# Kernel tuning notes

Hardware: AMD Instinct MI355X
Metric: run time of the kernel (lower is better)

Reference implementation:

```python
import jax, jax.numpy as jnp
import numpy as np

N = 50000      # nodes
E = 800000     # edges (avg degree 16)
DIN = 256      # input_dim
H = 4          # heads
C = 32         # output_dim per head
HID = H * C    # 128
NEG_SLOPE = 0.2


def setup_inputs() -> dict:
    key = jax.random.key(0)
    ks = jax.random.split(key, 12)
    s = 0.05
    d = {}
    d["x"] = jax.random.normal(ks[0], (N, DIN), jnp.float32)
    d["edge_index"] = jax.random.randint(ks[1], (2, E), 0, N, jnp.int32)
    # GATv2Conv layer 0 (in=DIN)
    d["Wl0"] = jax.random.normal(ks[2], (HID, DIN), jnp.float32) * s
    d["Wr0"] = jax.random.normal(ks[3], (HID, DIN), jnp.float32) * s
    d["att0"] = jax.random.normal(ks[4], (H, C), jnp.float32) * s
    d["b0"] = jnp.zeros((HID,), jnp.float32)
    # GATv2Conv layer 1 (in=HID)
    d["Wl1"] = jax.random.normal(ks[5], (HID, HID), jnp.float32) * s
    d["Wr1"] = jax.random.normal(ks[6], (HID, HID), jnp.float32) * s
    d["att1"] = jax.random.normal(ks[7], (H, C), jnp.float32) * s
    d["b1"] = jnp.zeros((HID,), jnp.float32)
    # down_proj: Linear(HID -> C)
    d["down_W"] = jax.random.normal(ks[8], (C, HID), jnp.float32) * s
    d["down_b"] = jnp.zeros((C,), jnp.float32)
    return d


def _gatv2_layer(x, src, dst, Wl, Wr, att, b, n):
    # x: [n, Din]; src/dst: [Etot] (self loops included)
    xl = (x @ Wl.T).reshape(n, H, C)   # messages (x_j side, lin_l)
    xr = (x @ Wr.T).reshape(n, H, C)   # target side (x_i, lin_r)
    e = jax.nn.leaky_relu(xl[src] + xr[dst], NEG_SLOPE)   # [Etot, H, C]
    logits = jnp.einsum('ehc,hc->eh', e, att)             # [Etot, H]
    # softmax over incoming edges per destination node
    m = jax.ops.segment_max(logits, dst, num_segments=n)
    ex = jnp.exp(logits - m[dst])
    den = jax.ops.segment_sum(ex, dst, num_segments=n)
    alpha = ex / den[dst]                                 # [Etot, H]
    out = jax.ops.segment_sum(alpha[:, :, None] * xl[src], dst, num_segments=n)
    return out.reshape(n, HID) + b                        # concat heads + bias


def reference(x, edge_index, Wl0, Wr0, att0, b0, Wl1, Wr1, att1, b1, down_W, down_b):
    n = x.shape[0]
    loops = jnp.arange(n, dtype=edge_index.dtype)
    ei = jnp.concatenate([edge_index, jnp.stack([loops, loops])], axis=1)  # add_self_loops=True
    src, dst = ei[0], ei[1]
    h = _gatv2_layer(x, src, dst, Wl0, Wr0, att0, b0, n)
    h = _gatv2_layer(h, src, dst, Wl1, Wr1, att1, b1, n)
    return h @ down_W.T + down_b    # down_proj: [n, C]
```

## Files before the change

kernel.cpp:

```cpp
#include <hip/hip_runtime.h>

#define CAP 64
#define BCAP 6144

typedef _Float16 h8 __attribute__((ext_vector_type(8)));
typedef _Float16 h4 __attribute__((ext_vector_type(4)));
typedef _Float16 h2 __attribute__((ext_vector_type(2)));
typedef float f32x4 __attribute__((ext_vector_type(4)));

__device__ __forceinline__ float lrelu(float x){ return x > 0.f ? x : 0.2f * x; }
__device__ __forceinline__ uint4 pack8(float4 a, float4 b){
  union { h8 h; uint4 u; } cv;
  cv.h = (h8){ (_Float16)a.x, (_Float16)a.y, (_Float16)a.z, (_Float16)a.w,
               (_Float16)b.x, (_Float16)b.y, (_Float16)b.z, (_Float16)b.w };
  return cv.u;
}

__device__ __forceinline__ float edge_logit(uint4 xu, const h2* xrh, const h2* avh){
  union { uint4 u; h2 v[4]; } cu; cu.u = xu;
  const h2 z2 = { (_Float16)0.f, (_Float16)0.f };
  const h2 sl = { (_Float16)0.2f, (_Float16)0.2f };
  float p = 0.f;
  #pragma unroll
  for (int k = 0; k < 4; ++k){
    h2 t  = cu.v[k] + xrh[k];
    h2 hi = __builtin_elementwise_max(t, z2);
    h2 lo = __builtin_elementwise_min(t, z2);
    h2 lr = hi + lo * sl;
    p = __builtin_amdgcn_fdot2(lr, avh[k], p, false);
  }
  return p;
}
__device__ __forceinline__ void acc_edge(float w, uint4 xu, float* accv){
  union { uint4 u; _Float16 e[8]; } ce; ce.u = xu;
  #pragma unroll
  for (int i = 0; i < 8; ++i) accv[i] += w * (float)ce.e[i];
}

__global__ void convw_kernel(const float* __restrict__ Wl0, const float* __restrict__ Wr0,
                             const float* __restrict__ Wl1, const float* __restrict__ Wr1,
                             _Float16* __restrict__ B0h, _Float16* __restrict__ B1h){
  int t = blockIdx.x * blockDim.x + threadIdx.x;
  const float* s; _Float16* d; int off;
  if (t < 8192)      { s = Wl0; d = B0h;          off = t; }
  else if (t < 16384){ s = Wr0; d = B0h + 32768;  off = t - 8192; }
  else if (t < 20480){ s = Wl1; d = B1h;          off = t - 16384; }
  else               { s = Wr1; d = B1h + 16384;  off = t - 20480; }
  float4 f = ((const float4*)s)[off];
  h4 h = { (_Float16)f.x, (_Float16)f.y, (_Float16)f.z, (_Float16)f.w };
  *(h4*)(d + 4 * (size_t)off) = h;
}

__global__ void scatter_kernel(const int* __restrict__ cnt, const int* __restrict__ hist,
                               int* __restrict__ cursor, int* __restrict__ perm, int n){
  __shared__ int base[64];
  __shared__ int lh[64];
  __shared__ int lbase[64];
  __shared__ int ht[64];
  if (threadIdx.x < 64){
    lh[threadIdx.x] = 0;
    ht[threadIdx.x] = hist[threadIdx.x];
  }
  __syncthreads();
  if (threadIdx.x == 0){
    int acc = 0;
    for (int d = 63; d >= 0; --d){ base[d] = acc; acc += ht[d]; }
  }
  int i = blockIdx.x * blockDim.x + threadIdx.x;
  int d = 1, lr = 0;
  if (i < n){
    d = cnt[i]; d = (d < 1) ? 1 : (d > CAP ? CAP : d);
    lr = atomicAdd(&lh[d - 1], 1);
  }
  __syncthreads();
  if (threadIdx.x < 64 && lh[threadIdx.x] > 0)
    lbase[threadIdx.x] = atomicAdd(&cursor[threadIdx.x], lh[threadIdx.x]);
  __syncthreads();
  if (i < n)
    perm[base[d - 1] + lbase[d - 1] + lr] = i;
}

__device__ __forceinline__ void gemm_body(
    char* smem, const float* __restrict__ A32, const _Float16* __restrict__ A16,
    const _Float16* __restrict__ Bw, _Float16* __restrict__ C, int n, int K,
    int bx, int by)
{
  char* Abase = smem;
  char* Bbase = smem + 8192;

  const int tid  = threadIdx.x;
  const int lane = tid & 63;
  const int wx   = tid >> 6;
  const int r0   = by * 64;
  const int cb   = bx * 128;
  const int m16  = lane & 15, quad = lane >> 4;

  f32x4 acc[4][2];
  #pragma unroll
  for (int i = 0; i < 4; ++i)
    #pragma unroll
    for (int j = 0; j < 2; ++j)
      acc[i][j] = (f32x4){0.f, 0.f, 0.f, 0.f};

  const int srow = tid >> 2;
  const int kq   = (tid & 3) << 4;
  const int kb   = kq * 2;
  const int swz  = (srow & 7) << 4;

  uint4 ra[2], rb[2][2];
  const uint4 z = {0u, 0u, 0u, 0u};

  if (r0 + srow < n){
    if (A32){
      const float* p = A32 + (size_t)(r0 + srow) * K + kq;
      ra[0] = pack8(*(const float4*)(p),     *(const float4*)(p + 4));
      ra[1] = pack8(*(const float4*)(p + 8), *(const float4*)(p + 12));
    } else {
      const _Float16* p = A16 + (size_t)(r0 + srow) * K + kq;
      ra[0] = *(const uint4*)(p);
      ra[1] = *(const uint4*)(p + 8);
    }
  } else { ra[0] = z; ra[1] = z; }
  #pragma unroll
  for (int v = 0; v < 2; ++v){
    const _Float16* p = Bw + (size_t)(cb + v * 64 + srow) * K + kq;
    rb[v][0] = *(const uint4*)(p);
    rb[v][1] = *(const uint4*)(p + 8);
  }

  const int nt = K >> 6;
  for (int t = 0; t < nt; ++t){
    *(uint4*)(Abase + srow * 128 + (kb ^ swz))        = ra[0];
    *(uint4*)(Abase + srow * 128 + ((kb + 16) ^ swz)) = ra[1];
    #pragma unroll
    for (int v = 0; v < 2; ++v){
      *(uint4*)(Bbase + (v * 64 + srow) * 128 + (kb ^ swz))        = rb[v][0];
      *(uint4*)(Bbase + (v * 64 + srow) * 128 + ((kb + 16) ^ swz)) = rb[v][1];
    }
    __syncthreads();
    if (t + 1 < nt){
      int kt = (t + 1) << 6;
      if (r0 + srow < n){
        if (A32){
          const float* p = A32 + (size_t)(r0 + srow) * K + kt + kq;
          ra[0] = pack8(*(const float4*)(p),     *(const float4*)(p + 4));
          ra[1] = pack8(*(const float4*)(p + 8), *(const float4*)(p + 12));
        } else {
          const _Float16* p = A16 + (size_t)(r0 + srow) * K + kt + kq;
          ra[0] = *(const uint4*)(p);
          ra[1] = *(const uint4*)(p + 8);
        }
      }
      #pragma unroll
      for (int v = 0; v < 2; ++v){
        const _Float16* p = Bw + (size_t)(cb + v * 64 + srow) * K + kt + kq;
        rb[v][0] = *(const uint4*)(p);
        rb[v][1] = *(const uint4*)(p + 8);
      }
    }
    const int swr = (m16 & 7) << 4;
    #pragma unroll
    for (int ks = 0; ks < 2; ++ks){
      const int k0 = ks * 32 + quad * 8;
      const int cbyte = (k0 * 2) ^ swr;
      h8 a[4], b[2];
      #pragma unroll
      for (int i = 0; i < 4; ++i)
        a[i] = *(const h8*)(Abase + (i * 16 + m16) * 128 + cbyte);
      #pragma unroll
      for (int j = 0; j < 2; ++j)
        b[j] = *(const h8*)(Bbase + (wx * 32 + j * 16 + m16) * 128 + cbyte);
      #pragma unroll
      for (int i = 0; i < 4; ++i)
        #pragma unroll
        for (int j = 0; j < 2; ++j)
          acc[i][j] = __builtin_amdgcn_mfma_f32_16x16x32_f16(a[i], b[j], acc[i][j], 0, 0, 0);
    }
    __syncthreads();
  }

  _Float16* Csm = (_Float16*)smem;
  #pragma unroll
  for (int i = 0; i < 4; ++i)
    #pragma unroll
    for (int r = 0; r < 4; ++r){
      int lrow = i * 16 + quad * 4 + r;
      _Float16* cp = Csm + lrow * 136 + wx * 32 + m16;
      #pragma unroll
      for (int j = 0; j < 2; ++j)
        cp[j * 16] = (_Float16)acc[i][j][r];
    }
  __syncthreads();
  #pragma unroll
  for (int v = 0; v < 4; ++v){
    int idx = v * 256 + tid;
    int row = idx >> 4, cx = (idx & 15) * 8;
    if (r0 + row < n)
      *(uint4*)(C + (size_t)(r0 + row) * 256 + cb + cx)
        = *(const uint4*)(Csm + row * 136 + cx);
  }
}

__global__ __launch_bounds__(256) void gemm_mfma(
    const float* __restrict__ A32, const _Float16* __restrict__ A16,
    const _Float16* __restrict__ Bw, _Float16* __restrict__ C, int n, int K)
{
  __shared__ __align__(16) char smem[24576];
  gemm_body(smem, A32, A16, Bw, C, n, K, blockIdx.x, blockIdx.y);
}

__global__ __launch_bounds__(256) void gemm_pass1(
    const float* __restrict__ A32, const _Float16* __restrict__ Bw,
    _Float16* __restrict__ C, int n,
    const int* __restrict__ ei, int* __restrict__ bins, int* __restrict__ bcursor,
    int e_orig, int etot, int NP)
{
  __shared__ __align__(16) char smem[24576];
  const int lin = blockIdx.x;
  if (lin >= NP){
    int gi = lin - NP;
    gemm_body(smem, A32, nullptr, Bw, C, n, 256, gi & 1, gi >> 1);
  } else {
    int* lcnt  = (int*)smem;
    int* gbase = lcnt + 256;
    const int tid = threadIdx.x;
    if (tid < 196) lcnt[tid] = 0;
    __syncthreads();
    const int base = lin * 2048 + tid;
    int pk[8], bk[8], lp[8];
    #pragma unroll
    for (int k = 0; k < 8; ++k){
      int i = base + k * 256;
      bk[k] = -1;
      if (i < etot){
        int src, dst;
        if (i < e_orig){ src = ei[i]; dst = ei[e_orig + i]; }
        else { src = i - e_orig; dst = src; }
        bk[k] = dst >> 8;
        pk[k] = ((dst & 255) << 24) | src;
      }
    }
    #pragma unroll
    for (int k = 0; k < 8; ++k)
      if (bk[k] >= 0) lp[k] = atomicAdd(&lcnt[bk[k]], 1);
    __syncthreads();
    if (tid < 196 && lcnt[tid] > 0)
      gbase[tid] = atomicAdd(&bcursor[tid], lcnt[tid]);
    __syncthreads();
    #pragma unroll
    for (int k = 0; k < 8; ++k)
      if (bk[k] >= 0){
        int p = gbase[bk[k]] + lp[k];
        if (p < BCAP) bins[(size_t)bk[k] * BCAP + p] = pk[k];
      }
  }
}

__global__ __launch_bounds__(256) void pass2_kernel(
    const int* __restrict__ bins, const int* __restrict__ bcursor,
    int* __restrict__ cnt, int* __restrict__ col2, int* __restrict__ hist, int n)
{
  __shared__ int stage[256 * CAP];
  __shared__ int lcnt2[256];
  __shared__ int lh[64];
  const int b = blockIdx.x, tid = threadIdx.x;
  lcnt2[tid] = 0;
  if (tid < 64) lh[tid] = 0;
  __syncthreads();
  int ecnt = bcursor[b]; if (ecnt > BCAP) ecnt = BCAP;
  for (int i = tid; i < ecnt; i += 256){
    int v = bins[(size_t)b * BCAP + i];
    int src = v & 0xFFFFFF;
    int loc = ((unsigned)v) >> 24;
    int pos = atomicAdd(&lcnt2[loc], 1);
    if (pos < CAP) stage[loc * CAP + pos] = src;
  }
  __syncthreads();
  int node = b * 256 + tid;
  if (node < n){
    int d = lcnt2[tid];
    cnt[node] = d;
    int dc = d < 1 ? 1 : (d > CAP ? CAP : d);
    atomicAdd(&lh[dc - 1], 1);
  }
  __syncthreads();
  const uint4* sg = (const uint4*)stage;
  uint4* c4 = (uint4*)col2;
  for (int k2 = tid; k2 < 4096; k2 += 256){
    int nd = b * 256 + (k2 >> 4);
    if (nd < n) c4[(size_t)nd * 16 + (k2 & 15)] = sg[k2];
  }
  if (tid < 64 && lh[tid] > 0) atomicAdd(&hist[tid], lh[tid]);
}

__global__ __launch_bounds__(128) void agg_wave(
    const _Float16* __restrict__ XLR, const int* __restrict__ col2,
    const int* __restrict__ cnt, const int* __restrict__ perm,
    const float* __restrict__ att,
    const float* __restrict__ bias, _Float16* __restrict__ H16, int n)
{
  __shared__ int idxs[8][72];
  const int lane  = threadIdx.x & 63;
  const int g     = lane >> 4;
  const int ll    = lane & 15;
  const int gbase = g << 4;
  const int nl    = ((threadIdx.x >> 6) << 2) + g;
  const int slot  = blockIdx.x * 8 + nl;
  if (slot >= n) return;
  const int node = perm[slot];
  int deg = cnt[node]; if (deg > CAP) deg = CAP;
  const int c0 = 8 * ll;

  h2 xrh[4], avh[4];
  {
    union { uint4 u; h2 v[4]; } xc;
    xc.u = *(const uint4*)(XLR + (size_t)node * 256 + 128 + c0);
    #pragma unroll
    for (int k = 0; k < 4; ++k) xrh[k] = xc.v[k];
    #pragma unroll
    for (int k = 0; k < 4; ++k)
      avh[k] = (h2){ (_Float16)att[c0 + 2*k], (_Float16)att[c0 + 2*k + 1] };
  }

  {
    int sq[4];
    #pragma unroll
    for (int q = 0; q < 4; ++q)
      sq[q] = (ll + 16*q < deg) ? col2[(size_t)node * CAP + ll + 16*q] : 0;
    int s0 = __shfl(sq[0], gbase);
    #pragma unroll
    for (int q = 0; q < 4; ++q)
      idxs[nl][ll + 16*q] = (ll + 16*q < deg) ? sq[q] : s0;
    if (ll < 8) idxs[nl][64 + ll] = s0;
  }
  const int* idxp = idxs[nl];

  float l = 0.f, accv[8];
  #pragma unroll
  for (int i = 0; i < 8; ++i) accv[i] = 0.f;

  uint4 x0, x1, x2, x3, x4, x5, x6, x7;
  {
    int e0 = idxp[0], e1 = idxp[1], e2 = idxp[2], e3 = idxp[3];
    int e4 = idxp[4], e5 = idxp[5], e6 = idxp[6], e7 = idxp[7];
    x0 = *(const uint4*)(XLR + (size_t)e0 * 256 + c0);
    x1 = *(const uint4*)(XLR + (size_t)e1 * 256 + c0);
    x2 = *(const uint4*)(XLR + (size_t)e2 * 256 + c0);
    x3 = *(const uint4*)(XLR + (size_t)e3 * 256 + c0);
    x4 = *(const uint4*)(XLR + (size_t)e4 * 256 + c0);
    x5 = *(const uint4*)(XLR + (size_t)e5 * 256 + c0);
    x6 = *(const uint4*)(XLR + (size_t)e6 * 256 + c0);
    x7 = *(const uint4*)(XLR + (size_t)e7 * 256 + c0);
  }

  int j = 0;
  for (; j + 4 <= deg; j += 4){
    uint4 y0 = x0, y1 = x1, y2 = x2, y3 = x3;
    x0 = x4; x1 = x5; x2 = x6; x3 = x7;
    int e8  = idxp[j + 8],  e9  = idxp[j + 9];
    int e10 = idxp[j + 10], e11 = idxp[j + 11];
    x4 = *(const uint4*)(XLR + (size_t)e8  * 256 + c0);
    x5 = *(const uint4*)(XLR + (size_t)e9  * 256 + c0);
    x6 = *(const uint4*)(XLR + (size_t)e10 * 256 + c0);
    x7 = *(const uint4*)(XLR + (size_t)e11 * 256 + c0);
    float p0 = edge_logit(y0, xrh, avh);
    float p1 = edge_logit(y1, xrh, avh);
    float p2 = edge_logit(y2, xrh, avh);
    float p3 = edge_logit(y3, xrh, avh);
    p0 += __shfl_xor(p0, 1);  p1 += __shfl_xor(p1, 1);
    p2 += __shfl_xor(p2, 1);  p3 += __shfl_xor(p3, 1);
    p0 += __shfl_xor(p0, 2);  p1 += __shfl_xor(p1, 2);
    p2 += __shfl_xor(p2, 2);  p3 += __shfl_xor(p3, 2);
    float w0 = __expf(p0), w1 = __expf(p1), w2 = __expf(p2), w3 = __expf(p3);
    l += (w0 + w1) + (w2 + w3);
    acc_edge(w0, y0, accv); acc_edge(w1, y1, accv);
    acc_edge(w2, y2, accv); acc_edge(w3, y3, accv);
  }
  #pragma unroll
  for (int r = 0; r < 3; ++r){
    if (j + r < deg){
      uint4 xe = (r == 0) ? x0 : ((r == 1) ? x1 : x2);
      float p = edge_logit(xe, xrh, avh);
      p += __shfl_xor(p, 1);
      p += __shfl_xor(p, 2);
      float w = __expf(p);
      l += w;
      acc_edge(w, xe, accv);
    }
  }
  float inv = 1.f / l;
  union { h8 h; uint4 u; } o;
  #pragma unroll
  for (int i = 0; i < 8; ++i)
    o.h[i] = (_Float16)(accv[i] * inv + bias[c0 + i]);
  *(uint4*)(H16 + (size_t)node * 128 + c0) = o.u;
}

__global__ __launch_bounds__(256) void agg_down(
    const _Float16* __restrict__ XLR, const int* __restrict__ col2,
    const int* __restrict__ cnt, const int* __restrict__ perm,
    const float* __restrict__ att,
    const float* __restrict__ bias, const float* __restrict__ dW,
    const float* __restrict__ db, float* __restrict__ out, int n)
{
  __shared__ float dwb[32][129];
  __shared__ float hsm[16][128];
  __shared__ int idxs[16][72];
  for (int i = threadIdx.x; i < 32 * 128; i += 256)
    dwb[i >> 7][i & 127] = dW[i];

  const int lane  = threadIdx.x & 63;
  const int g     = lane >> 4;
  const int ll    = lane & 15;
  const int gbase = g << 4;
  const int nl    = ((threadIdx.x >> 6) << 2) + g;
  const int slot  = blockIdx.x * 16 + nl;
  const bool valid = slot < n;
  const int node = valid ? perm[slot] : 0;
  int deg = 0;
  if (valid){ deg = cnt[node]; if (deg > CAP) deg = CAP; }
  const int c0 = 8 * ll;

  h2 xrh[4], avh[4];
  {
    union { uint4 u; h2 v[4]; } xc;
    xc.u = (uint4){0u,0u,0u,0u};
    if (valid) xc.u = *(const uint4*)(XLR + (size_t)node * 256 + 128 + c0);
    #pragma unroll
    for (int k = 0; k < 4; ++k) xrh[k] = xc.v[k];
    #pragma unroll
    for (int k = 0; k < 4; ++k)
      avh[k] = (h2){ (_Float16)att[c0 + 2*k], (_Float16)att[c0 + 2*k + 1] };
  }

  {
    int sq[4];
    #pragma unroll
    for (int q = 0; q < 4; ++q)
      sq[q] = (valid && ll + 16*q < deg) ? col2[(size_t)node * CAP + ll + 16*q] : 0;
    int s0 = __shfl(sq[0], gbase);
    #pragma unroll
    for (int q = 0; q < 4; ++q)
      idxs[nl][ll + 16*q] = (ll + 16*q < deg) ? sq[q] : s0;
    if (ll < 8) idxs[nl][64 + ll] = s0;
  }
  const int* idxp = idxs[nl];

  float l = 0.f, accv[8];
  #pragma unroll
  for (int i = 0; i < 8; ++i) accv[i] = 0.f;

  uint4 x0, x1, x2, x3, x4, x5, x6, x7;
  {
    int e0 = idxp[0], e1 = idxp[1], e2 = idxp[2], e3 = idxp[3];
    int e4 = idxp[4], e5 = idxp[5], e6 = idxp[6], e7 = idxp[7];
    x0 = *(const uint4*)(XLR + (size_t)e0 * 256 + c0);
    x1 = *(const uint4*)(XLR + (size_t)e1 * 256 + c0);
    x2 = *(const uint4*)(XLR + (size_t)e2 * 256 + c0);
    x3 = *(const uint4*)(XLR + (size_t)e3 * 256 + c0);
    x4 = *(const uint4*)(XLR + (size_t)e4 * 256 + c0);
    x5 = *(const uint4*)(XLR + (size_t)e5 * 256 + c0);
    x6 = *(const uint4*)(XLR + (size_t)e6 * 256 + c0);
    x7 = *(const uint4*)(XLR + (size_t)e7 * 256 + c0);
  }

  int j = 0;
  for (; j + 4 <= deg; j += 4){
    uint4 y0 = x0, y1 = x1, y2 = x2, y3 = x3;
    x0 = x4; x1 = x5; x2 = x6; x3 = x7;
    int e8  = idxp[j + 8],  e9  = idxp[j + 9];
    int e10 = idxp[j + 10], e11 = idxp[j + 11];
    x4 = *(const uint4*)(XLR + (size_t)e8  * 256 + c0);
    x5 = *(const uint4*)(XLR + (size_t)e9  * 256 + c0);
    x6 = *(const uint4*)(XLR + (size_t)e10 * 256 + c0);
    x7 = *(const uint4*)(XLR + (size_t)e11 * 256 + c0);
    float p0 = edge_logit(y0, xrh, avh);
    float p1 = edge_logit(y1, xrh, avh);
    float p2 = edge_logit(y2, xrh, avh);
    float p3 = edge_logit(y3, xrh, avh);
    p0 += __shfl_xor(p0, 1);  p1 += __shfl_xor(p1, 1);
    p2 += __shfl_xor(p2, 1);  p3 += __shfl_xor(p3, 1);
    p0 += __shfl_xor(p0, 2);  p1 += __shfl_xor(p1, 2);
    p2 += __shfl_xor(p2, 2);  p3 += __shfl_xor(p3, 2);
    float w0 = __expf(p0), w1 = __expf(p1), w2 = __expf(p2), w3 = __expf(p3);
    l += (w0 + w1) + (w2 + w3);
    acc_edge(w0, y0, accv); acc_edge(w1, y1, accv);
    acc_edge(w2, y2, accv); acc_edge(w3, y3, accv);
  }
  #pragma unroll
  for (int r = 0; r < 3; ++r){
    if (j + r < deg){
      uint4 xe = (r == 0) ? x0 : ((r == 1) ? x1 : x2);
      float p = edge_logit(xe, xrh, avh);
      p += __shfl_xor(p, 1);
      p += __shfl_xor(p, 2);
      float w = __expf(p);
      l += w;
      acc_edge(w, xe, accv);
    }
  }
  {
    float inv = (deg > 0) ? 1.f / l : 0.f;
    #pragma unroll
    for (int i = 0; i < 8; ++i)
      hsm[nl][c0 + i] = accv[i] * inv + bias[c0 + i];
  }
  __syncthreads();

  const int o = threadIdx.x & 31;
  #pragma unroll
  for (int h2i = 0; h2i < 2; ++h2i){
    int nl2 = (threadIdx.x >> 5) + h2i * 8;
    int slot2 = blockIdx.x * 16 + nl2;
    float sum = 0.f;
    #pragma unroll 8
    for (int k = 0; k < 128; ++k)
      sum += hsm[nl2][k] * dwb[o][k];
    if (slot2 < n)
      out[(size_t)perm[slot2] * 32 + o] = sum + db[o];
  }
}

extern "C" void kernel_launch(void* const* d_in, const int* in_sizes, int n_in,
                              void* d_out, int out_size, void* d_ws, size_t ws_size,
                              hipStream_t stream) {
  const float* x     = (const float*)d_in[0];
  const int*   ei    = (const int*)  d_in[1];
  const float* Wl0   = (const float*)d_in[2];
  const float* Wr0   = (const float*)d_in[3];
  const float* att0  = (const float*)d_in[4];
  const float* b0    = (const float*)d_in[5];
  const float* Wl1   = (const float*)d_in[6];
  const float* Wr1   = (const float*)d_in[7];
  const float* att1  = (const float*)d_in[8];
  const float* b1    = (const float*)d_in[9];
  const float* dW    = (const float*)d_in[10];
  const float* db    = (const float*)d_in[11];
  float* out = (float*)d_out;

  const int n    = in_sizes[0] / 256;
  const int e    = in_sizes[1] / 2;
  const int etot = e + n;

  _Float16* XLR16 = (_Float16*)d_ws;
  _Float16* H16   = XLR16 + (size_t)n * 256;
  int* col2 = (int*)(H16 + (size_t)n * 128);
  int* cnt  = col2 + (size_t)n * CAP;
  int* hist    = cnt + n;
  int* cursor  = hist + 64;
  int* bcursor = cursor + 64;
  int* perm    = bcursor + 256;
  _Float16* B0h = (_Float16*)(perm + ((n + 3) & ~3));
  _Float16* B1h = B0h + 65536;
  int* bins = (int*)H16;

  (void)hipMemsetAsync(cnt, 0, ((size_t)n + 384) * sizeof(int), stream);
  convw_kernel<<<96, 256, 0, stream>>>(Wl0, Wr0, Wl1, Wr1, B0h, B1h);

  const int NP = (etot + 2047) / 2048;
  const int NG = 2 * ((n + 63) / 64);
  gemm_pass1<<<NP + NG, 256, 0, stream>>>(x, B0h, XLR16, n, ei, bins, bcursor,
                                          e, etot, NP);

  const int NB2 = (n + 255) / 256;
  pass2_kernel<<<NB2, 256, 0, stream>>>(bins, bcursor, cnt, col2, hist, n);
  scatter_kernel<<<(n + 255) / 256, 256, 0, stream>>>(cnt, hist, cursor, perm, n);

  agg_wave<<<(n + 7) / 8, 128, 0, stream>>>(XLR16, col2, cnt, perm, att0, b0, H16, n);
  dim3 ggrid(2, (n + 63) / 64);
  gemm_mfma<<<ggrid, 256, 0, stream>>>(nullptr, H16, B1h, XLR16, n, 128);
  agg_down<<<(n + 15) / 16, 256, 0, stream>>>(XLR16, col2, cnt, perm, att1, b1, dW, db, out, n);
}
```

Measured before the change: 274.5 us.

## Fuse layer-0 aggregation with layer-1 GEMM in permuted slot order

Replaces the separate layer-0 aggregation kernel and layer-1 GEMM with a single kernel that aggregates 64 nodes into shared memory and multiplies them by the layer-1 weights with MFMA. The H16 intermediate round-trip and one launch go away. The layer-1 features are now stored in degree-sorted slot order, so an inverse permutation is built in the scatter kernel and used by the second aggregation to remap neighbour indices. The fused kernel uses about 53KB of shared memory, which lowers occupancy, and the second aggregation pays an extra indirect load per edge.

```diff
diff --git a/kernel.cpp b/kernel.cpp
--- a/kernel.cpp
+++ b/kernel.cpp
@@ -8,7 +8,6 @@
 typedef _Float16 h2 __attribute__((ext_vector_type(2)));
 typedef float f32x4 __attribute__((ext_vector_type(4)));
 
-__device__ __forceinline__ float lrelu(float x){ return x > 0.f ? x : 0.2f * x; }
 __device__ __forceinline__ uint4 pack8(float4 a, float4 b){
   union { h8 h; uint4 u; } cv;
   cv.h = (h8){ (_Float16)a.x, (_Float16)a.y, (_Float16)a.z, (_Float16)a.w,
@@ -52,7 +51,8 @@
 }
 
 __global__ void scatter_kernel(const int* __restrict__ cnt, const int* __restrict__ hist,
-                               int* __restrict__ cursor, int* __restrict__ perm, int n){
+                               int* __restrict__ cursor, int* __restrict__ perm,
+                               int* __restrict__ iperm, int n){
   __shared__ int base[64];
   __shared__ int lh[64];
   __shared__ int lbase[64];
@@ -76,12 +76,15 @@
   if (threadIdx.x < 64 && lh[threadIdx.x] > 0)
     lbase[threadIdx.x] = atomicAdd(&cursor[threadIdx.x], lh[threadIdx.x]);
   __syncthreads();
-  if (i < n)
-    perm[base[d - 1] + lbase[d - 1] + lr] = i;
+  if (i < n){
+    int pos = base[d - 1] + lbase[d - 1] + lr;
+    perm[pos] = i;
+    iperm[i] = pos;
+  }
 }
 
 __device__ __forceinline__ void gemm_body(
-    char* smem, const float* __restrict__ A32, const _Float16* __restrict__ A16,
+    char* smem, const float* __restrict__ A32,
     const _Float16* __restrict__ Bw, _Float16* __restrict__ C, int n, int K,
     int bx, int by)
 {
@@ -111,15 +114,9 @@
   const uint4 z = {0u, 0u, 0u, 0u};
 
   if (r0 + srow < n){
-    if (A32){
-      const float* p = A32 + (size_t)(r0 + srow) * K + kq;
-      ra[0] = pack8(*(const float4*)(p),     *(const float4*)(p + 4));
-      ra[1] = pack8(*(const float4*)(p + 8), *(const float4*)(p + 12));
-    } else {
-      const _Float16* p = A16 + (size_t)(r0 + srow) * K + kq;
-      ra[0] = *(const uint4*)(p);
-      ra[1] = *(const uint4*)(p + 8);
-    }
+    const float* p = A32 + (size_t)(r0 + srow) * K + kq;
+    ra[0] = pack8(*(const float4*)(p),     *(const float4*)(p + 4));
+    ra[1] = pack8(*(const float4*)(p + 8), *(const float4*)(p + 12));
   } else { ra[0] = z; ra[1] = z; }
   #pragma unroll
   for (int v = 0; v < 2; ++v){
@@ -141,15 +138,9 @@
     if (t + 1 < nt){
       int kt = (t + 1) << 6;
       if (r0 + srow < n){
-        if (A32){
-          const float* p = A32 + (size_t)(r0 + srow) * K + kt + kq;
-          ra[0] = pack8(*(const float4*)(p),     *(const float4*)(p + 4));
-          ra[1] = pack8(*(const float4*)(p + 8), *(const float4*)(p + 12));
-        } else {
-          const _Float16* p = A16 + (size_t)(r0 + srow) * K + kt + kq;
-          ra[0] = *(const uint4*)(p);
-          ra[1] = *(const uint4*)(p + 8);
-        }
+        const float* p = A32 + (size_t)(r0 + srow) * K + kt + kq;
+        ra[0] = pack8(*(const float4*)(p),     *(const float4*)(p + 4));
+        ra[1] = pack8(*(const float4*)(p + 8), *(const float4*)(p + 12));
       }
       #pragma unroll
       for (int v = 0; v < 2; ++v){
@@ -199,14 +190,6 @@
       *(uint4*)(C + (size_t)(r0 + row) * 256 + cb + cx)
         = *(const uint4*)(Csm + row * 136 + cx);
   }
-}
-
-__global__ __launch_bounds__(256) void gemm_mfma(
-    const float* __restrict__ A32, const _Float16* __restrict__ A16,
-    const _Float16* __restrict__ Bw, _Float16* __restrict__ C, int n, int K)
-{
-  __shared__ __align__(16) char smem[24576];
-  gemm_body(smem, A32, A16, Bw, C, n, K, blockIdx.x, blockIdx.y);
 }
 
 __global__ __launch_bounds__(256) void gemm_pass1(
@@ -219,7 +202,7 @@
   const int lin = blockIdx.x;
   if (lin >= NP){
     int gi = lin - NP;
-    gemm_body(smem, A32, nullptr, Bw, C, n, 256, gi & 1, gi >> 1);
+    gemm_body(smem, A32, Bw, C, n, 256, gi & 1, gi >> 1);
   } else {
     int* lcnt  = (int*)smem;
     int* gbase = lcnt + 256;
@@ -293,112 +276,210 @@
   if (tid < 64 && lh[tid] > 0) atomicAdd(&hist[tid], lh[tid]);
 }
 
-__global__ __launch_bounds__(128) void agg_wave(
+__global__ __launch_bounds__(256) void agg_gemm1(
     const _Float16* __restrict__ XLR, const int* __restrict__ col2,
     const int* __restrict__ cnt, const int* __restrict__ perm,
-    const float* __restrict__ att,
-    const float* __restrict__ bias, _Float16* __restrict__ H16, int n)
+    const float* __restrict__ att, const float* __restrict__ bias,
+    const _Float16* __restrict__ B1h, _Float16* __restrict__ XLR1, int n)
 {
-  __shared__ int idxs[8][72];
-  const int lane  = threadIdx.x & 63;
-  const int g     = lane >> 4;
-  const int ll    = lane & 15;
-  const int gbase = g << 4;
-  const int nl    = ((threadIdx.x >> 6) << 2) + g;
-  const int slot  = blockIdx.x * 8 + nl;
-  if (slot >= n) return;
-  const int node = perm[slot];
-  int deg = cnt[node]; if (deg > CAP) deg = CAP;
+  __shared__ __align__(16) char smem[53760];
+  char* Hs = smem;
+  char* Bs = smem + 16384;
+  int (*idxs)[72] = (int(*)[72])(smem + 49152);
+
+  const int tid  = threadIdx.x;
+  const int lane = tid & 63;
+  const int g = lane >> 4, ll = lane & 15, gbase = g << 4;
+  const int nlq = ((tid >> 6) << 2) + g;
+  const int slot0 = blockIdx.x * 64;
   const int c0 = 8 * ll;
 
-  h2 xrh[4], avh[4];
+  for (int rnd = 0; rnd < 4; ++rnd){
+    const int lrow = rnd * 16 + nlq;
+    const int slot = slot0 + lrow;
+    const bool valid = slot < n;
+    const int node = valid ? perm[slot] : 0;
+    int deg = 0;
+    if (valid){ deg = cnt[node]; if (deg > CAP) deg = CAP; }
+
+    h2 xrh[4], avh[4];
+    {
+      union { uint4 u; h2 v[4]; } xc;
+      xc.u = (uint4){0u,0u,0u,0u};
+      if (valid) xc.u = *(const uint4*)(XLR + (size_t)node * 256 + 128 + c0);
+      #pragma unroll
+      for (int k = 0; k < 4; ++k) xrh[k] = xc.v[k];
+      #pragma unroll
+      for (int k = 0; k < 4; ++k)
+        avh[k] = (h2){ (_Float16)att[c0 + 2*k], (_Float16)att[c0 + 2*k + 1] };
+    }
+    {
+      int sq[4];
+      #pragma unroll
+      for (int q = 0; q < 4; ++q)
+        sq[q] = (valid && ll + 16*q < deg) ? col2[(size_t)node * CAP + ll + 16*q] : 0;
+      int s0 = __shfl(sq[0], gbase);
+      #pragma unroll
+      for (int q = 0; q < 4; ++q)
+        idxs[nlq][ll + 16*q] = (ll + 16*q < deg) ? sq[q] : s0;
+      if (ll < 8) idxs[nlq][64 + ll] = s0;
+    }
+    const int* idxp = idxs[nlq];
+
+    float l = 0.f, accv[8];
+    #pragma unroll
+    for (int i = 0; i < 8; ++i) accv[i] = 0.f;
+
+    uint4 x0, x1, x2, x3, x4, x5, x6, x7;
+    {
+      int e0 = idxp[0], e1 = idxp[1], e2 = idxp[2], e3 = idxp[3];
+      int e4 = idxp[4], e5 = idxp[5], e6 = idxp[6], e7 = idxp[7];
+      x0 = *(const uint4*)(XLR + (size_t)e0 * 256 + c0);
+      x1 = *(const uint4*)(XLR + (size_t)e1 * 256 + c0);
+      x2 = *(const uint4*)(XLR + (size_t)e2 * 256 + c0);
+      x3 = *(const uint4*)(XLR + (size_t)e3 * 256 + c0);
+      x4 = *(const uint4*)(XLR + (size_t)e4 * 256 + c0);
+      x5 = *(const uint4*)(XLR + (size_t)e5 * 256 + c0);
+      x6 = *(const uint4*)(XLR + (size_t)e6 * 256 + c0);
+      x7 = *(const uint4*)(XLR + (size_t)e7 * 256 + c0);
+    }
+
+    int j = 0;
+    for (; j + 4 <= deg; j += 4){
+      uint4 y0 = x0, y1 = x1, y2 = x2, y3 = x3;
+      x0 = x4; x1 = x5; x2 = x6; x3 = x7;
+      int e8  = idxp[j + 8],  e9  = idxp[j + 9];
+      int e10 = idxp[j + 10], e11 = idxp[j + 11];
+      x4 = *(const uint4*)(XLR + (size_t)e8  * 256 + c0);
+      x5 = *(const uint4*)(XLR + (size_t)e9  * 256 + c0);
+      x6 = *(const uint4*)(XLR + (size_t)e10 * 256 + c0);
+      x7 = *(const uint4*)(XLR + (size_t)e11 * 256 + c0);
+      float p0 = edge_logit(y0, xrh, avh);
+      float p1 = edge_logit(y1, xrh, avh);
+      float p2 = edge_logit(y2, xrh, avh);
+      float p3 = edge_logit(y3, xrh, avh);
+      p0 += __shfl_xor(p0, 1);  p1 += __shfl_xor(p1, 1);
+      p2 += __shfl_xor(p2, 1);  p3 += __shfl_xor(p3, 1);
+      p0 += __shfl_xor(p0, 2);  p1 += __shfl_xor(p1, 2);
+      p2 += __shfl_xor(p2, 2);  p3 += __shfl_xor(p3, 2);
+      float w0 = __expf(p0), w1 = __expf(p1), w2 = __expf(p2), w3 = __expf(p3);
+      l += (w0 + w1) + (w2 + w3);
+      acc_edge(w0, y0, accv); acc_edge(w1, y1, accv);
+      acc_edge(w2, y2, accv); acc_edge(w3, y3, accv);
+    }
+    #pragma unroll
+    for (int r = 0; r < 3; ++r){
+      if (j + r < deg){
+        uint4 xe = (r == 0) ? x0 : ((r == 1) ? x1 : x2);
+        float p = edge_logit(xe, xrh, avh);
+        p += __shfl_xor(p, 1);
+        p += __shfl_xor(p, 2);
+        float w = __expf(p);
+        l += w;
+        acc_edge(w, xe, accv);
+      }
+    }
+    if (valid){
+      float inv = (deg > 0) ? 1.f / l : 0.f;
+      union { h8 h; uint4 u; } o;
+      #pragma unroll
+      for (int i = 0; i < 8; ++i)
+        o.h[i] = (_Float16)(accv[i] * inv + bias[c0 + i]);
+      *(uint4*)(Hs + lrow * 256 + ((c0 * 2) ^ ((lrow & 7) << 4))) = o.u;
+    }
+  }
+  __syncthreads();
+
+  const int wx = tid >> 6;
+  const int m16 = lane & 15, quad = lane >> 4;
+  const int swr = (m16 & 7) << 4;
+  f32x4 acc[4][4];
+  #pragma unroll
+  for (int i = 0; i < 4; ++i)
+    #pragma unroll
+    for (int j = 0; j < 4; ++j)
+      acc[i][j] = (f32x4){0.f, 0.f, 0.f, 0.f};
+
+  uint4 rbf[8];
   {
-    union { uint4 u; h2 v[4]; } xc;
-    xc.u = *(const uint4*)(XLR + (size_t)node * 256 + 128 + c0);
-    #pragma unroll
-    for (int k = 0; k < 4; ++k) xrh[k] = xc.v[k];
-    #pragma unroll
-    for (int k = 0; k < 4; ++k)
-      avh[k] = (h2){ (_Float16)att[c0 + 2*k], (_Float16)att[c0 + 2*k + 1] };
-  }
-
+    const _Float16* p = B1h + (size_t)tid * 128;
+    #pragma unroll
+    for (int k = 0; k < 8; ++k) rbf[k] = *(const uint4*)(p + k * 8);
+  }
+  #pragma unroll
+  for (int k = 0; k < 8; ++k)
+    *(uint4*)(Bs + tid * 128 + ((k * 16) ^ ((tid & 7) << 4))) = rbf[k];
+  __syncthreads();
   {
-    int sq[4];
-    #pragma unroll
-    for (int q = 0; q < 4; ++q)
-      sq[q] = (ll + 16*q < deg) ? col2[(size_t)node * CAP + ll + 16*q] : 0;
-    int s0 = __shfl(sq[0], gbase);
-    #pragma unroll
-    for (int q = 0; q < 4; ++q)
-      idxs[nl][ll + 16*q] = (ll + 16*q < deg) ? sq[q] : s0;
-    if (ll < 8) idxs[nl][64 + ll] = s0;
-  }
-  const int* idxp = idxs[nl];
-
-  float l = 0.f, accv[8];
-  #pragma unroll
-  for (int i = 0; i < 8; ++i) accv[i] = 0.f;
-
-  uint4 x0, x1, x2, x3, x4, x5, x6, x7;
-  {
-    int e0 = idxp[0], e1 = idxp[1], e2 = idxp[2], e3 = idxp[3];
-    int e4 = idxp[4], e5 = idxp[5], e6 = idxp[6], e7 = idxp[7];
-    x0 = *(const uint4*)(XLR + (size_t)e0 * 256 + c0);
-    x1 = *(const uint4*)(XLR + (size_t)e1 * 256 + c0);
-    x2 = *(const uint4*)(XLR + (size_t)e2 * 256 + c0);
-    x3 = *(const uint4*)(XLR + (size_t)e3 * 256 + c0);
-    x4 = *(const uint4*)(XLR + (size_t)e4 * 256 + c0);
-    x5 = *(const uint4*)(XLR + (size_t)e5 * 256 + c0);
-    x6 = *(const uint4*)(XLR + (size_t)e6 * 256 + c0);
-    x7 = *(const uint4*)(XLR + (size_t)e7 * 256 + c0);
-  }
-
-  int j = 0;
-  for (; j + 4 <= deg; j += 4){
-    uint4 y0 = x0, y1 = x1, y2 = x2, y3 = x3;
-    x0 = x4; x1 = x5; x2 = x6; x3 = x7;
-    int e8  = idxp[j + 8],  e9  = idxp[j + 9];
-    int e10 = idxp[j + 10], e11 = idxp[j + 11];
-    x4 = *(const uint4*)(XLR + (size_t)e8  * 256 + c0);
-    x5 = *(const uint4*)(XLR + (size_t)e9  * 256 + c0);
-    x6 = *(const uint4*)(XLR + (size_t)e10 * 256 + c0);
-    x7 = *(const uint4*)(XLR + (size_t)e11 * 256 + c0);
-    float p0 = edge_logit(y0, xrh, avh);
-    float p1 = edge_logit(y1, xrh, avh);
-    float p2 = edge_logit(y2, xrh, avh);
-    float p3 = edge_logit(y3, xrh, avh);
-    p0 += __shfl_xor(p0, 1);  p1 += __shfl_xor(p1, 1);
-    p2 += __shfl_xor(p2, 1);  p3 += __shfl_xor(p3, 1);
-    p0 += __shfl_xor(p0, 2);  p1 += __shfl_xor(p1, 2);
-    p2 += __shfl_xor(p2, 2);  p3 += __shfl_xor(p3, 2);
-    float w0 = __expf(p0), w1 = __expf(p1), w2 = __expf(p2), w3 = __expf(p3);
-    l += (w0 + w1) + (w2 + w3);
-    acc_edge(w0, y0, accv); acc_edge(w1, y1, accv);
-    acc_edge(w2, y2, accv); acc_edge(w3, y3, accv);
-  }
-  #pragma unroll
-  for (int r = 0; r < 3; ++r){
-    if (j + r < deg){
-      uint4 xe = (r == 0) ? x0 : ((r == 1) ? x1 : x2);
-      float p = edge_logit(xe, xrh, avh);
-      p += __shfl_xor(p, 1);
-      p += __shfl_xor(p, 2);
-      float w = __expf(p);
-      l += w;
-      acc_edge(w, xe, accv);
-    }
-  }
-  float inv = 1.f / l;
-  union { h8 h; uint4 u; } o;
-  #pragma unroll
-  for (int i = 0; i < 8; ++i)
-    o.h[i] = (_Float16)(accv[i] * inv + bias[c0 + i]);
-  *(uint4*)(H16 + (size_t)node * 128 + c0) = o.u;
+    const _Float16* p = B1h + (size_t)tid * 128 + 64;
+    #pragma unroll
+    for (int k = 0; k < 8; ++k) rbf[k] = *(const uint4*)(p + k * 8);
+  }
+  #pragma unroll
+  for (int ks = 0; ks < 2; ++ks){
+    const int kw = ks * 32 + quad * 8;
+    h8 a[4], b[4];
+    #pragma unroll
+    for (int i = 0; i < 4; ++i)
+      a[i] = *(const h8*)(Hs + (i * 16 + m16) * 256 + ((kw * 2) ^ swr));
+    #pragma unroll
+    for (int j = 0; j < 4; ++j)
+      b[j] = *(const h8*)(Bs + (wx * 64 + j * 16 + m16) * 128 + ((kw * 2) ^ swr));
+    #pragma unroll
+    for (int i = 0; i < 4; ++i)
+      #pragma unroll
+      for (int j = 0; j < 4; ++j)
+        acc[i][j] = __builtin_amdgcn_mfma_f32_16x16x32_f16(a[i], b[j], acc[i][j], 0, 0, 0);
+  }
+  __syncthreads();
+  #pragma unroll
+  for (int k = 0; k < 8; ++k)
+    *(uint4*)(Bs + tid * 128 + ((k * 16) ^ ((tid & 7) << 4))) = rbf[k];
+  __syncthreads();
+  #pragma unroll
+  for (int ks = 0; ks < 2; ++ks){
+    const int kw = ks * 32 + quad * 8;
+    h8 a[4], b[4];
+    #pragma unroll
+    for (int i = 0; i < 4; ++i)
+      a[i] = *(const h8*)(Hs + (i * 16 + m16) * 256 + (((64 + kw) * 2) ^ swr));
+    #pragma unroll
+    for (int j = 0; j < 4; ++j)
+      b[j] = *(const h8*)(Bs + (wx * 64 + j * 16 + m16) * 128 + ((kw * 2) ^ swr));
+    #pragma unroll
+    for (int i = 0; i < 4; ++i)
+      #pragma unroll
+      for (int j = 0; j < 4; ++j)
+        acc[i][j] = __builtin_amdgcn_mfma_f32_16x16x32_f16(a[i], b[j], acc[i][j], 0, 0, 0);
+  }
+  __syncthreads();
+
+  _Float16* Csm = (_Float16*)smem;
+  #pragma unroll
+  for (int i = 0; i < 4; ++i)
+    #pragma unroll
+    for (int r = 0; r < 4; ++r){
+      int lrow = i * 16 + quad * 4 + r;
+      _Float16* cp = Csm + lrow * 264 + wx * 64 + m16;
+      #pragma unroll
+      for (int j = 0; j < 4; ++j)
+        cp[j * 16] = (_Float16)acc[i][j][r];
+    }
+  __syncthreads();
+  #pragma unroll
+  for (int v = 0; v < 8; ++v){
+    int idx = v * 256 + tid;
+    int row = idx >> 5, cx = (idx & 31) * 8;
+    if (slot0 + row < n)
+      *(uint4*)(XLR1 + (size_t)(slot0 + row) * 256 + cx)
+        = *(const uint4*)(Csm + row * 264 + cx);
+  }
 }
 
 __global__ __launch_bounds__(256) void agg_down(
-    const _Float16* __restrict__ XLR, const int* __restrict__ col2,
+    const _Float16* __restrict__ XLR1, const int* __restrict__ col2,
     const int* __restrict__ cnt, const int* __restrict__ perm,
+    const int* __restrict__ iperm,
     const float* __restrict__ att,
     const float* __restrict__ bias, const float* __restrict__ dW,
     const float* __restrict__ db, float* __restrict__ out, int n)
@@ -425,7 +506,7 @@
   {
     union { uint4 u; h2 v[4]; } xc;
     xc.u = (uint4){0u,0u,0u,0u};
-    if (valid) xc.u = *(const uint4*)(XLR + (size_t)node * 256 + 128 + c0);
+    if (valid) xc.u = *(const uint4*)(XLR1 + (size_t)slot * 256 + 128 + c0);
     #pragma unroll
     for (int k = 0; k < 4; ++k) xrh[k] = xc.v[k];
     #pragma unroll
@@ -437,7 +518,8 @@
     int sq[4];
     #pragma unroll
     for (int q = 0; q < 4; ++q)
-      sq[q] = (valid && ll + 16*q < deg) ? col2[(size_t)node * CAP + ll + 16*q] : 0;
+      sq[q] = (valid && ll + 16*q < deg)
+                ? iperm[col2[(size_t)node * CAP + ll + 16*q]] : 0;
     int s0 = __shfl(sq[0], gbase);
     #pragma unroll
     for (int q = 0; q < 4; ++q)
@@ -454,14 +536,14 @@
   {
     int e0 = idxp[0], e1 = idxp[1], e2 = idxp[2], e3 = idxp[3];
     int e4 = idxp[4], e5 = idxp[5], e6 = idxp[6], e7 = idxp[7];
-    x0 = *(const uint4*)(XLR + (size_t)e0 * 256 + c0);
-    x1 = *(const uint4*)(XLR + (size_t)e1 * 256 + c0);
-    x2 = *(const uint4*)(XLR + (size_t)e2 * 256 + c0);
-    x3 = *(const uint4*)(XLR + (size_t)e3 * 256 + c0);
-    x4 = *(const uint4*)(XLR + (size_t)e4 * 256 + c0);
-    x5 = *(const uint4*)(XLR + (size_t)e5 * 256 + c0);
-    x6 = *(const uint4*)(XLR + (size_t)e6 * 256 + c0);
-    x7 = *(const uint4*)(XLR + (size_t)e7 * 256 + c0);
+    x0 = *(const uint4*)(XLR1 + (size_t)e0 * 256 + c0);
+    x1 = *(const uint4*)(XLR1 + (size_t)e1 * 256 + c0);
+    x2 = *(const uint4*)(XLR1 + (size_t)e2 * 256 + c0);
+    x3 = *(const uint4*)(XLR1 + (size_t)e3 * 256 + c0);
+    x4 = *(const uint4*)(XLR1 + (size_t)e4 * 256 + c0);
+    x5 = *(const uint4*)(XLR1 + (size_t)e5 * 256 + c0);
+    x6 = *(const uint4*)(XLR1 + (size_t)e6 * 256 + c0);
+    x7 = *(const uint4*)(XLR1 + (size_t)e7 * 256 + c0);
   }
 
   int j = 0;
@@ -470,10 +552,10 @@
     x0 = x4; x1 = x5; x2 = x6; x3 = x7;
     int e8  = idxp[j + 8],  e9  = idxp[j + 9];
     int e10 = idxp[j + 10], e11 = idxp[j + 11];
-    x4 = *(const uint4*)(XLR + (size_t)e8  * 256 + c0);
-    x5 = *(const uint4*)(XLR + (size_t)e9  * 256 + c0);
-    x6 = *(const uint4*)(XLR + (size_t)e10 * 256 + c0);
-    x7 = *(const uint4*)(XLR + (size_t)e11 * 256 + c0);
+    x4 = *(const uint4*)(XLR1 + (size_t)e8  * 256 + c0);
+    x5 = *(const uint4*)(XLR1 + (size_t)e9  * 256 + c0);
+    x6 = *(const uint4*)(XLR1 + (size_t)e10 * 256 + c0);
+    x7 = *(const uint4*)(XLR1 + (size_t)e11 * 256 + c0);
     float p0 = edge_logit(y0, xrh, avh);
     float p1 = edge_logit(y1, xrh, avh);
     float p2 = edge_logit(y2, xrh, avh);
@@ -543,16 +625,17 @@
   const int etot = e + n;
 
   _Float16* XLR16 = (_Float16*)d_ws;
-  _Float16* H16   = XLR16 + (size_t)n * 256;
-  int* col2 = (int*)(H16 + (size_t)n * 128);
+  _Float16* XLR1  = XLR16 + (size_t)n * 256;
+  int* col2 = (int*)(XLR1 + (size_t)n * 256);
   int* cnt  = col2 + (size_t)n * CAP;
   int* hist    = cnt + n;
   int* cursor  = hist + 64;
   int* bcursor = cursor + 64;
   int* perm    = bcursor + 256;
-  _Float16* B0h = (_Float16*)(perm + ((n + 3) & ~3));
+  int* iperm   = perm + n;
+  _Float16* B0h = (_Float16*)(iperm + ((n + 3) & ~3));
   _Float16* B1h = B0h + 65536;
-  int* bins = (int*)H16;
+  int* bins = (int*)XLR1;
 
   (void)hipMemsetAsync(cnt, 0, ((size_t)n + 384) * sizeof(int), stream);
   convw_kernel<<<96, 256, 0, stream>>>(Wl0, Wr0, Wl1, Wr1, B0h, B1h);
@@ -564,10 +647,10 @@
 
   const int NB2 = (n + 255) / 256;
   pass2_kernel<<<NB2, 256, 0, stream>>>(bins, bcursor, cnt, col2, hist, n);
-  scatter_kernel<<<(n + 255) / 256, 256, 0, stream>>>(cnt, hist, cursor, perm, n);
-
-  agg_wave<<<(n + 7) / 8, 128, 0, stream>>>(XLR16, col2, cnt, perm, att0, b0, H16, n);
-  dim3 ggrid(2, (n + 63) / 64);
-  gemm_mfma<<<ggrid, 256, 0, stream>>>(nullptr, H16, B1h, XLR16, n, 128);
-  agg_down<<<(n + 15) / 16, 256, 0, stream>>>(XLR16, col2, cnt, perm, att1, b1, dW, db, out, n);
-}
+  scatter_kernel<<<(n + 255) / 256, 256, 0, stream>>>(cnt, hist, cursor, perm, iperm, n);
+
+  agg_gemm1<<<(n + 63) / 64, 256, 0, stream>>>(XLR16, col2, cnt, perm, att0, b0,
+                                               B1h, XLR1, n);
+  agg_down<<<(n + 15) / 16, 256, 0, stream>>>(XLR1, col2, cnt, perm, iperm,
+                                              att1, b1, dW, db, out, n);
+}
```

After: 301.4 us. 1.1x slower.
